# Optimization experiments

Measured on AMD Instinct MI355X. Metric: run time of the kernel, lower is better.

Reference implementation:

```python
import jax, jax.numpy as jnp
import numpy as np


def _causal_kernel_mask(K):
    # casual_mask[i, K-i:] = 0 for i in 1..p
    p = K // 2
    m = np.ones((p + 1, K), np.float32)
    for i in range(1, p + 1):
        m[i, K - i:] = 0.0
    return jnp.asarray(m)


def setup_inputs() -> dict:
    rng = jax.random.key(0)
    k0, k1, k2, k3, k4 = jax.random.split(rng, 5)
    B, H, N, F = 2, 16, 1024, 64
    V, K = 32000, 5
    return {
        "input_ids": jax.random.randint(k0, (B, N), 0, V),
        "query": jax.random.normal(k1, (B, H, N, F), dtype=jnp.float32),
        "key": jax.random.normal(k2, (B, H, N, F), dtype=jnp.float32),
        "value": jax.random.normal(k3, (B, H, N, F), dtype=jnp.float32),
        "emb_weight": jax.random.normal(k4, (V, 2 * K), dtype=jnp.float32) * 0.02,
    }


def reference(input_ids, query, key, value, emb_weight):
    B, H, N, F = query.shape
    K = emb_weight.shape[1] // 2  # head/layer invariant -> emb dim = 2*K
    p = K // 2
    G = 2 * H

    # ---- get_kernel (layer 0; head_invariant + layer_invariant) ----
    kern = emb_weight[input_ids]                       # [B,N,2K]
    kern = kern.reshape(B, N, 2, 1, K)                 # [B,N,2,1,K]
    kern = jnp.broadcast_to(kern, (B, N, 2, H, K)).reshape(B, N, G, K)

    # ---- conv_key_value (for_casual=True, strict_on_casual=True) ----
    kv = jnp.concatenate([key, value], axis=1)         # [B,2H,N,F]
    kv_pad = jnp.pad(kv, ((0, 0), (0, 0), (p, p), (0, 0)))
    # unfold over token dim: [B,2H,K,N,F]
    kv_unf = jnp.stack([kv_pad[:, :, k:k + N, :] for k in range(K)], axis=2)
    cmask = _causal_kernel_mask(K)                     # [p+1,K]
    kern_m = kern[:, :, :, None, :] * cmask[None, None, None]  # [B,N,2H,p+1,K]
    # dynamic depthwise conv with per-offset causal masking
    out = jnp.einsum('bgknf,bngjk->bgjnf', kv_unf, kern_m)     # [B,2H,p+1,N,F]
    key_c = out[:, :H, 0]                              # [B,H,N,F]
    value_c = out[:, H:, 0]                            # [B,H,N,F]

    # ---- attention with causal-boundary corrections (n_past = 0) ----
    scale = 1.0 / jnp.sqrt(jnp.asarray(F, dtype=query.dtype))
    q = query * scale
    scores = jnp.einsum('bhnf,bhmf->bhnm', q, key_c)   # [B,H,N,N]

    # correct_attn_weights_near_casual_boundary
    for i in range(p):
        off = p - 1 - i
        cb_key = out[:, :H, 1 + i]                     # [B,H,N,F]
        corr = jnp.einsum('bhnf,bhnf->bhn', q[:, :, off:, :], cb_key[:, :, :N - off, :])
        rows = jnp.arange(N - off) + off
        cols = jnp.arange(N - off)
        scores = scores.at[:, :, rows, cols].set(corr)

    causal = jnp.tril(jnp.ones((N, N), dtype=bool))
    scores = jnp.where(causal, scores, jnp.asarray(-1e9, dtype=scores.dtype))
    probs = jax.nn.softmax(scores, axis=-1)
    attn = jnp.einsum('bhnm,bhmf->bhnf', probs, value_c)

    # correct_attn_output_near_casual_boundary
    for i in range(p):
        off = p - 1 - i
        cb_value = out[:, H:, 1 + i]                   # [B,H,N,F]
        idx = jnp.arange(N - off)
        diag_w = probs[:, :, idx + off, idx]           # diag offset=-off: [B,H,N-off]
        diff_v = cb_value[:, :, :N - off, :] - value_c[:, :, :N - off, :]
        diff = diag_w[..., None] * diff_v
        attn = attn + jnp.pad(diff, ((0, 0), (0, 0), (off, 0), (0, 0)))

    return attn
```

## Files before the change

### kernel.cpp

```cpp
#include <hip/hip_runtime.h>

#define HD    64
#define NSEQ  1024
#define NPB   12
#define CROWS 32
#define LOG2E 1.44269504088896f

typedef __attribute__((ext_vector_type(8))) __bf16 bf16x8;
typedef __attribute__((ext_vector_type(4))) float  f32x4;
typedef __attribute__((ext_vector_type(4))) unsigned short u16x4;

__device__ __constant__ unsigned char PAIRS12[NPB] = {
    6, 8, 10, 12, 14, 15, 4, 13, 2, 11, 0, 9 };

__device__ inline unsigned short f2bf(float x) {
    unsigned u = __float_as_uint(x);
    return (unsigned short)((u + 0x7fffu + ((u >> 16) & 1u)) >> 16);
}
__device__ inline unsigned pk2(float a, float b) {
    return (unsigned)f2bf(a) | ((unsigned)f2bf(b) << 16);
}
__device__ inline float dot4(f32x4 a, f32x4 b) {
    return a.x * b.x + a.y * b.y + a.z * b.z + a.w * b.w;
}

__global__ __launch_bounds__(256) void conv_kernel(
    const int* __restrict__ ids,
    const float* __restrict__ keyg,
    const float* __restrict__ valg,
    const float* __restrict__ qg,
    const float* __restrict__ emb,
    unsigned short* __restrict__ kc,
    unsigned short* __restrict__ vcT,
    float* __restrict__ dg1, float* __restrict__ dg2)
{
    __shared__ float se[(CROWS + 1) * 10];
    __shared__ float vtile[CROWS][68];
    int pid = blockIdx.x;
    int bh = pid & 31;
    int n0 = (pid >> 5) * CROWS;
    int b  = bh >> 4;
    int t  = threadIdx.x;
    size_t hb = (size_t)bh * NSEQ * HD;

    for (int u = t; u < (CROWS + 1) * 10; u += 256) {
        int r = u / 10, c = u - r * 10;
        int n = n0 - 1 + r;
        se[u] = (n >= 0) ? emb[(size_t)ids[b * NSEQ + n] * 10 + c] : 0.f;
    }
    __syncthreads();

    const float* kb = keyg + hb;
    const float* vb = valg + hb;
#pragma unroll
    for (int i = 0; i < 2; ++i) {
        int u  = (i << 8) + t;
        int nl = u >> 4, g4 = u & 15;
        int n  = n0 + nl, f = g4 << 2;
        const float* e  = se + (nl + 1) * 10;
        const float* ep = se + nl * 10;
        f32x4 xk[5], xv[5];
#pragma unroll
        for (int k = 0; k < 5; ++k) {
            int m = n + k - 2;
            if (m >= 0 && m < NSEQ) {
                xk[k] = *(const f32x4*)(kb + (size_t)m * HD + f);
                xv[k] = *(const f32x4*)(vb + (size_t)m * HD + f);
            } else {
                xk[k] = (f32x4){0.f, 0.f, 0.f, 0.f};
                xv[k] = (f32x4){0.f, 0.f, 0.f, 0.f};
            }
        }
        f32x4 km3 = (n >= 3) ? *(const f32x4*)(kb + (size_t)(n - 3) * HD + f)
                             : (f32x4){0.f, 0.f, 0.f, 0.f};
        f32x4 qv = *(const f32x4*)(qg + hb + (size_t)n * HD + f) * (0.125f * LOG2E);

        f32x4 k012 = e[0] * xk[0] + e[1] * xk[1] + e[2] * xk[2];
        f32x4 kcv  = k012 + e[3] * xk[3] + e[4] * xk[4];
        f32x4 vcv  = e[5] * xv[0] + e[6] * xv[1] + e[7] * xv[2] + e[8] * xv[3] + e[9] * xv[4];

        u16x4 kq;
        kq.x = f2bf(kcv.x); kq.y = f2bf(kcv.y); kq.z = f2bf(kcv.z); kq.w = f2bf(kcv.w);
        *(u16x4*)(kc + hb + (size_t)n * HD + f) = kq;
        *(f32x4*)(&vtile[nl][f]) = vcv;

        float s2 = dot4(qv, k012);
        f32x4 kj1 = ep[0] * km3 + ep[1] * xk[0] + ep[2] * xk[1] + ep[3] * xk[2];
        float s1 = dot4(qv, kj1);
#pragma unroll
        for (int o = 1; o < 16; o <<= 1) {
            s2 += __shfl_xor(s2, o, 64);
            s1 += __shfl_xor(s1, o, 64);
        }
        if (g4 == 0) {
            dg2[bh * NSEQ + n] = s2;
            dg1[bh * NSEQ + n] = s1;
        }
    }
    __syncthreads();
#pragma unroll
    for (int i = 0; i < 2; ++i) {
        int u = (i << 8) + t;
        int f = u >> 3, nn = (u & 7) << 2;
        u16x4 o;
        o.x = f2bf(vtile[nn + 0][f]);
        o.y = f2bf(vtile[nn + 1][f]);
        o.z = f2bf(vtile[nn + 2][f]);
        o.w = f2bf(vtile[nn + 3][f]);
        *(u16x4*)(vcT + ((size_t)bh * HD + f) * NSEQ + n0 + nn) = o;
    }
}

__global__ __launch_bounds__(512, 4) void attn_kernel(
    const float* __restrict__ qg,
    const unsigned short* __restrict__ kc,
    const unsigned short* __restrict__ vcT,
    const float* __restrict__ dg1, const float* __restrict__ dg2,
    const float* __restrict__ valg, const int* __restrict__ ids,
    const float* __restrict__ emb,
    float* __restrict__ pML, unsigned short* __restrict__ pO,
    float* __restrict__ outg)
{
    __shared__ __align__(16) unsigned char sK[2][8192];
    __shared__ __align__(16) unsigned char sV[2][8192];
    __shared__ __align__(16) unsigned char sP[16384];

    int pid  = blockIdx.x;
    int bh   = pid & 31;
    int slot = pid >> 5;
    int code = PAIRS12[slot];
    int jj = code >> 1, cch = code & 1;
    int t0 = cch << 3;
    int ntile = 2 * jj + 2;
    int len = cch ? (ntile - 8) : (ntile > 8 ? 8 : ntile);

    int t = threadIdx.x;
    int wv = t >> 6, l = t & 63;
    int w_in = wv & 3;
    int my_j = 2 * jj + (wv >> 2);
    int nc  = (my_j >= 8) ? 2 : 1;
    int lq = l & 15, h = l >> 4, l7 = l & 7;
    int lid = h * 16 + lq;
    int qbw = my_j * 64 + w_in * 16;
    size_t hb = (size_t)bh * NSEQ * HD;

    const unsigned short* kcb = kc  + hb;
    const unsigned short* vtb = vcT + (size_t)bh * HD * NSEQ;

    bf16x8 qb0, qb1;
    {
        const float* qr = qg + hb + (size_t)(qbw + lq) * HD + 8 * h;
        f32x4 a0 = *(const f32x4*)(qr);
        f32x4 a1 = *(const f32x4*)(qr + 4);
        f32x4 b0 = *(const f32x4*)(qr + 32);
        f32x4 b1 = *(const f32x4*)(qr + 36);
        const float S = 0.125f * LOG2E;
        union { unsigned u[4]; bf16x8 v; } u0, u1;
        u0.u[0] = pk2(a0.x * S, a0.y * S); u0.u[1] = pk2(a0.z * S, a0.w * S);
        u0.u[2] = pk2(a1.x * S, a1.y * S); u0.u[3] = pk2(a1.z * S, a1.w * S);
        u1.u[0] = pk2(b0.x * S, b0.y * S); u1.u[1] = pk2(b0.z * S, b0.w * S);
        u1.u[2] = pk2(b1.x * S, b1.y * S); u1.u[3] = pk2(b1.z * S, b1.w * S);
        qb0 = u0.v; qb1 = u1.v;
    }
    float diag2_l = dg2[bh * NSEQ + qbw + lq];
    float diag1_l = dg1[bh * NSEQ + qbw + lq];

    f32x4 of[4];
#pragma unroll
    for (int ft = 0; ft < 4; ++ft) of[ft] = (f32x4){0.f, 0.f, 0.f, 0.f};
    float m_run = -1e30f, denom = 0.f;

    const int ka_off0 = ((0 + h) ^ l7) << 4;
    const int ka_off1 = ((4 + h) ^ l7) << 4;
    const int pr_base = wv * 2048 + lq * 128;
    const int chk0 = ((qbw > 0 ? qbw - 1 : 0) >> 6);

    const int s_r0 = (t & 511) >> 3, s_c0 = t & 7;
    const int s_cs0 = s_c0 ^ (s_r0 & 7);
    const int s_buf0 = t >> 9;
    const int s_r1 = ((t + 512) & 511) >> 3, s_c1 = (t + 512) & 7;
    const int s_cs1 = s_c1 ^ (s_r1 & 7);
    const int s_buf1 = (t + 512) >> 9;

    uint4 pf[2];
    auto issue = [&](int tg) {
        int kv0 = tg << 6;
        pf[0] = (s_buf0 == 0)
            ? *(const uint4*)(kcb + (size_t)(kv0 + s_r0) * HD + s_cs0 * 8)
            : *(const uint4*)(vtb + (size_t)s_r0 * NSEQ + kv0 + s_cs0 * 8);
        pf[1] = (s_buf1 == 0)
            ? *(const uint4*)(kcb + (size_t)(kv0 + s_r1) * HD + s_cs1 * 8)
            : *(const uint4*)(vtb + (size_t)s_r1 * NSEQ + kv0 + s_cs1 * 8);
    };
    auto commit = [&](int cu) {
        *(uint4*)((s_buf0 ? sV[cu] : sK[cu]) + s_r0 * 128 + s_c0 * 16) = pf[0];
        *(uint4*)((s_buf1 ? sV[cu] : sK[cu]) + s_r1 * 128 + s_c1 * 16) = pf[1];
    };

    issue(t0); commit(0);
    if (len > 1) issue(t0 + 1);
    __syncthreads();

    for (int ti = 0; ti < len; ++ti) {
        int cur = ti & 1;
        if (ti + 1 < len) commit(cur ^ 1);
        if (ti + 2 < len) issue(t0 + ti + 2);
        int tg  = t0 + ti;
        int kv0 = tg << 6;
        bool act = (tg <= my_j);

        if (act) {
            const unsigned char* sKc = sK[cur];
            const unsigned char* sVc = sV[cur];
            f32x4 p[4];
            __builtin_amdgcn_s_setprio(1);
#pragma unroll
            for (int st = 0; st < 4; ++st) {
                bf16x8 ka0 = *(const bf16x8*)(sKc + st * 2048 + lq * 128 + ka_off0);
                bf16x8 ka1 = *(const bf16x8*)(sKc + st * 2048 + lq * 128 + ka_off1);
                f32x4 d = (f32x4){0.f, 0.f, 0.f, 0.f};
                d = __builtin_amdgcn_mfma_f32_16x16x32_bf16(ka0, qb0, d, 0, 0, 0);
                d = __builtin_amdgcn_mfma_f32_16x16x32_bf16(ka1, qb1, d, 0, 0, 0);
                p[st] = d;
            }
            __builtin_amdgcn_s_setprio(0);

            if (tg >= chk0) {
                int n_l = qbw + lq;
#pragma unroll
                for (int st = 0; st < 4; ++st)
#pragma unroll
                    for (int r = 0; r < 4; ++r) {
                        int kv = kv0 + st * 16 + 4 * h + r;
                        float dd = p[st][r];
                        if (kv > n_l)           dd = -1e30f;
                        else if (kv == n_l)     dd = diag2_l;
                        else if (kv == n_l - 1) dd = diag1_l;
                        p[st][r] = dd;
                    }
            }

            float tmax = -1e30f;
#pragma unroll
            for (int st = 0; st < 4; ++st)
#pragma unroll
                for (int r = 0; r < 4; ++r) tmax = fmaxf(tmax, p[st][r]);
            tmax = fmaxf(tmax, __shfl_xor(tmax, 16, 64));
            tmax = fmaxf(tmax, __shfl_xor(tmax, 32, 64));
            if (!__all(tmax <= m_run + 7.0f)) {
                float m_new = fmaxf(m_run, tmax);
                float alpha = __builtin_exp2f(m_run - m_new);
                denom *= alpha;
                m_run = m_new;
#pragma unroll
                for (int r = 0; r < 4; ++r) {
                    float ar = __shfl(alpha, 4 * h + r, 64);
                    of[0][r] *= ar; of[1][r] *= ar; of[2][r] *= ar; of[3][r] *= ar;
                }
            }
            float lsum = 0.f;
#pragma unroll
            for (int st = 0; st < 4; ++st)
#pragma unroll
                for (int r = 0; r < 4; ++r) {
                    float e = __builtin_exp2f(p[st][r] - m_run);
                    p[st][r] = e;
                    lsum += e;
                }
            lsum += __shfl_xor(lsum, 16, 64);
            lsum += __shfl_xor(lsum, 32, 64);
            denom += lsum;

#pragma unroll
            for (int st = 0; st < 4; ++st) {
                uint2 uu;
                uu.x = pk2(p[st][0], p[st][1]);
                uu.y = pk2(p[st][2], p[st][3]);
                int chunk = (st << 1) + (h >> 1);
                *(uint2*)(sP + pr_base + ((chunk ^ l7) << 4) + ((h & 1) << 3)) = uu;
            }
            asm volatile("s_waitcnt lgkmcnt(0)" ::: "memory");
            __builtin_amdgcn_sched_barrier(0);

            __builtin_amdgcn_s_setprio(1);
#pragma unroll
            for (int kk = 0; kk < 2; ++kk) {
                int koff = kk ? ka_off1 : ka_off0;
                bf16x8 pa = *(const bf16x8*)(sP + pr_base + koff);
#pragma unroll
                for (int ft = 0; ft < 4; ++ft) {
                    bf16x8 vb = *(const bf16x8*)(sVc + ft * 2048 + lq * 128 + koff);
                    of[ft] = __builtin_amdgcn_mfma_f32_16x16x32_bf16(pa, vb, of[ft], 0, 0, 0);
                }
            }
            __builtin_amdgcn_s_setprio(0);
        }
        if (ti + 1 < len) __syncthreads();
    }

    int psBase = ((bh << 4) | my_j) << 2;
    if (nc > 1) {
        if (h == 0) {
            float2 ml; ml.x = m_run; ml.y = denom;
            *(float2*)(pML + ((size_t)(psBase + cch) * 64 + w_in * 16 + lq) * 2) = ml;
        }
#pragma unroll
        for (int ft = 0; ft < 4; ++ft)
#pragma unroll
            for (int r = 0; r < 4; ++r)
                pO[(size_t)((((psBase + cch) * 4 + w_in) * 4 + ft) * 4 + r) * 64 + lid] =
                    f2bf(of[ft][r]);
        return;
    }

    const float* vraw = valg + hb;
    float* outr = outg + hb;
    const int* idb = ids + (size_t)(bh >> 4) * NSEQ;
#pragma unroll
    for (int r = 0; r < 4; ++r) {
        int qrow = 4 * h + r;
        int n = qbw + qrow;
        float dn = __shfl(denom,   qrow, 64);
        float mf = __shfl(m_run,   qrow, 64);
        float d2 = __shfl(diag2_l, qrow, 64);
        float d1 = __shfl(diag1_l, qrow, 64);
        float inv = 1.0f / dn;
        float p2 = __builtin_exp2f(d2 - mf) * inv;
        float p1 = (n >= 1) ? __builtin_exp2f(d1 - mf) * inv : 0.f;
        int id_n = idb[n];
        float e8  = emb[(size_t)id_n * 10 + 8];
        float e9  = emb[(size_t)id_n * 10 + 9];
        float e9p = (n >= 1) ? emb[(size_t)idb[n - 1] * 10 + 9] : 0.f;
        float ca = -(p2 * e8 + p1 * e9p);
        float cb = -p2 * e9;
#pragma unroll
        for (int ft = 0; ft < 4; ++ft) {
            int f = ft * 16 + lq;
            float v = of[ft][r] * inv;
            if (n + 1 < NSEQ) v += ca * vraw[(size_t)(n + 1) * HD + f];
            if (n + 2 < NSEQ) v += cb * vraw[(size_t)(n + 2) * HD + f];
            outr[(size_t)n * HD + f] = v;
        }
    }
}

__global__ __launch_bounds__(256) void merge_kernel(
    const float* __restrict__ pML, const unsigned short* __restrict__ pO,
    const float* __restrict__ dg1, const float* __restrict__ dg2,
    const float* __restrict__ valg, const int* __restrict__ ids,
    const float* __restrict__ emb, float* __restrict__ outg)
{
    int pid = blockIdx.x;
    int bh = pid & 31, j = (pid >> 5) + 8;
    int t = threadIdx.x;
    int rloc = t >> 2, fg = t & 3;
    int n = (j << 6) + rloc;
    int f0 = fg << 4;
    size_t hb = (size_t)bh * NSEQ * HD;
    int psBase = ((bh << 4) | j) << 2;

    float mc[2], lc[2];
#pragma unroll
    for (int c = 0; c < 2; ++c) {
        float2 v = *(const float2*)(pML + ((size_t)(psBase + c) * 64 + rloc) * 2);
        mc[c] = v.x; lc[c] = v.y;
    }
    float mg = fmaxf(mc[0], mc[1]);
    float D = 0.f;
    f32x4 a0 = (f32x4){0.f,0.f,0.f,0.f}, a1 = a0, a2 = a0, a3 = a0;
#pragma unroll
    for (int c = 0; c < 2; ++c) {
        float wc = __builtin_exp2f(mc[c] - mg);
        D += lc[c] * wc;
        const unsigned short* pp = pO +
            (size_t)((((psBase + c) * 4 + (rloc >> 4)) * 4 + fg) * 4 + (rloc & 3)) * 64
            + ((rloc >> 2) & 3) * 16;
        uint4 ua = *(const uint4*)(pp);
        uint4 ub = *(const uint4*)(pp + 8);
        a0.x += wc * __uint_as_float(ua.x << 16);
        a0.y += wc * __uint_as_float(ua.x & 0xffff0000u);
        a0.z += wc * __uint_as_float(ua.y << 16);
        a0.w += wc * __uint_as_float(ua.y & 0xffff0000u);
        a1.x += wc * __uint_as_float(ua.z << 16);
        a1.y += wc * __uint_as_float(ua.z & 0xffff0000u);
        a1.z += wc * __uint_as_float(ua.w << 16);
        a1.w += wc * __uint_as_float(ua.w & 0xffff0000u);
        a2.x += wc * __uint_as_float(ub.x << 16);
        a2.y += wc * __uint_as_float(ub.x & 0xffff0000u);
        a2.z += wc * __uint_as_float(ub.y << 16);
        a2.w += wc * __uint_as_float(ub.y & 0xffff0000u);
        a3.x += wc * __uint_as_float(ub.z << 16);
        a3.y += wc * __uint_as_float(ub.z & 0xffff0000u);
        a3.z += wc * __uint_as_float(ub.w << 16);
        a3.w += wc * __uint_as_float(ub.w & 0xffff0000u);
    }
    float inv = 1.0f / D;
    float d2 = dg2[bh * NSEQ + n], d1 = dg1[bh * NSEQ + n];
    float p2 = __builtin_exp2f(d2 - mg) * inv;
    float p1 = __builtin_exp2f(d1 - mg) * inv;
    const int* idb = ids + (size_t)(bh >> 4) * NSEQ;
    int id_n = idb[n];
    float e8  = emb[(size_t)id_n * 10 + 8];
    float e9  = emb[(size_t)id_n * 10 + 9];
    float e9p = emb[(size_t)idb[n - 1] * 10 + 9];
    float ca = -(p2 * e8 + p1 * e9p);
    float cb = -p2 * e9;

    a0 *= inv; a1 *= inv; a2 *= inv; a3 *= inv;
    if (n + 1 < NSEQ) {
        const float* v1 = valg + hb + (size_t)(n + 1) * HD + f0;
        a0 += ca * *(const f32x4*)(v1);
        a1 += ca * *(const f32x4*)(v1 + 4);
        a2 += ca * *(const f32x4*)(v1 + 8);
        a3 += ca * *(const f32x4*)(v1 + 12);
    }
    if (n + 2 < NSEQ) {
        const float* v2 = valg + hb + (size_t)(n + 2) * HD + f0;
        a0 += cb * *(const f32x4*)(v2);
        a1 += cb * *(const f32x4*)(v2 + 4);
        a2 += cb * *(const f32x4*)(v2 + 8);
        a3 += cb * *(const f32x4*)(v2 + 12);
    }
    float* o = outg + hb + (size_t)n * HD + f0;
    *(f32x4*)(o)      = a0;
    *(f32x4*)(o + 4)  = a1;
    *(f32x4*)(o + 8)  = a2;
    *(f32x4*)(o + 12) = a3;
}

extern "C" void kernel_launch(void* const* d_in, const int* in_sizes, int n_in,
                              void* d_out, int out_size, void* d_ws, size_t ws_size,
                              hipStream_t stream)
{
    const int*   ids = (const int*)  d_in[0];
    const float* q   = (const float*)d_in[1];
    const float* key = (const float*)d_in[2];
    const float* val = (const float*)d_in[3];
    const float* emb = (const float*)d_in[4];
    float* out = (float*)d_out;

    char* w = (char*)d_ws;
    unsigned short* kc  = (unsigned short*)(w);
    unsigned short* vcT = (unsigned short*)(w + (4u << 20));
    float* dg1 = (float*)(w + 8388608);
    float* dg2 = (float*)(w + 8519680);
    float* pML = (float*)(w + 8650752);
    unsigned short* pO = (unsigned short*)(w + 9699328);

    conv_kernel<<<1024, 256, 0, stream>>>(ids, key, val, q, emb, kc, vcT, dg1, dg2);
    attn_kernel<<<32 * NPB, 512, 0, stream>>>(q, kc, vcT, dg1, dg2, val, ids, emb,
                                              pML, pO, out);
    merge_kernel<<<256, 256, 0, stream>>>(pML, pO, dg1, dg2, val, ids, emb, out);
}
```

Before: 54.84 us.

## Stage key/value halo tiles in shared memory and widen conv blocks to 64 rows

The conv kernel now loads each block's 64-row key and value tile, plus a 3-row halo, into shared memory once. The 5-tap convolution then reads its neighbours from LDS instead of issuing up to six redundant global loads per row. Blocks cover 64 rows instead of 32, so the grid is halved and halo overhead is amortised. In exchange the kernel uses more LDS (about 40KB per block), has fewer blocks, and adds an extra barrier to reuse the key buffer for the value transpose.

```diff
diff --git a/kernel.cpp b/kernel.cpp
--- a/kernel.cpp
+++ b/kernel.cpp
@@ -3,7 +3,6 @@
 #define HD    64
 #define NSEQ  1024
 #define NPB   12
-#define CROWS 32
 #define LOG2E 1.44269504088896f
 
 typedef __attribute__((ext_vector_type(8))) __bf16 bf16x8;
@@ -34,58 +33,72 @@
     unsigned short* __restrict__ vcT,
     float* __restrict__ dg1, float* __restrict__ dg2)
 {
-    __shared__ float se[(CROWS + 1) * 10];
-    __shared__ float vtile[CROWS][68];
+    __shared__ __align__(16) float sA[70 * 68];
+    __shared__ __align__(16) float sB[70 * 68];
+    __shared__ float sE[65 * 10];
+
     int pid = blockIdx.x;
     int bh = pid & 31;
-    int n0 = (pid >> 5) * CROWS;
+    int n0 = (pid >> 5) << 6;
     int b  = bh >> 4;
     int t  = threadIdx.x;
     size_t hb = (size_t)bh * NSEQ * HD;
-
-    for (int u = t; u < (CROWS + 1) * 10; u += 256) {
+    const float* kb = keyg + hb;
+    const float* vb = valg + hb;
+
+    for (int u = t; u < 650; u += 256) {
         int r = u / 10, c = u - r * 10;
         int n = n0 - 1 + r;
-        se[u] = (n >= 0) ? emb[(size_t)ids[b * NSEQ + n] * 10 + c] : 0.f;
+        sE[u] = (n >= 0) ? emb[(size_t)ids[b * NSEQ + n] * 10 + c] : 0.f;
+    }
+    for (int u = t; u < 70 * 16; u += 256) {
+        int r = u >> 4, f = (u & 15) << 2;
+        int g = n0 - 3 + r;
+        f32x4 kv4 = (f32x4){0.f, 0.f, 0.f, 0.f};
+        f32x4 vv4 = (f32x4){0.f, 0.f, 0.f, 0.f};
+        if (g >= 0 && g < NSEQ) {
+            kv4 = *(const f32x4*)(kb + (size_t)g * HD + f);
+            vv4 = *(const f32x4*)(vb + (size_t)g * HD + f);
+        }
+        *(f32x4*)(sA + r * 68 + f) = kv4;
+        *(f32x4*)(sB + r * 68 + f) = vv4;
     }
     __syncthreads();
 
-    const float* kb = keyg + hb;
-    const float* vb = valg + hb;
-#pragma unroll
-    for (int i = 0; i < 2; ++i) {
+    f32x4 vcv_save[4];
+#pragma unroll
+    for (int i = 0; i < 4; ++i) {
         int u  = (i << 8) + t;
         int nl = u >> 4, g4 = u & 15;
         int n  = n0 + nl, f = g4 << 2;
-        const float* e  = se + (nl + 1) * 10;
-        const float* ep = se + nl * 10;
-        f32x4 xk[5], xv[5];
-#pragma unroll
-        for (int k = 0; k < 5; ++k) {
-            int m = n + k - 2;
-            if (m >= 0 && m < NSEQ) {
-                xk[k] = *(const f32x4*)(kb + (size_t)m * HD + f);
-                xv[k] = *(const f32x4*)(vb + (size_t)m * HD + f);
-            } else {
-                xk[k] = (f32x4){0.f, 0.f, 0.f, 0.f};
-                xv[k] = (f32x4){0.f, 0.f, 0.f, 0.f};
-            }
-        }
-        f32x4 km3 = (n >= 3) ? *(const f32x4*)(kb + (size_t)(n - 3) * HD + f)
-                             : (f32x4){0.f, 0.f, 0.f, 0.f};
+        const float* e  = sE + (nl + 1) * 10;
+        const float* ep = sE + nl * 10;
+        const float* ar = sA + nl * 68 + f;
+        const float* br = sB + nl * 68 + f;
+        f32x4 km3 = *(const f32x4*)(ar);
+        f32x4 x0 = *(const f32x4*)(ar + 68);
+        f32x4 x1 = *(const f32x4*)(ar + 2 * 68);
+        f32x4 x2 = *(const f32x4*)(ar + 3 * 68);
+        f32x4 x3 = *(const f32x4*)(ar + 4 * 68);
+        f32x4 x4 = *(const f32x4*)(ar + 5 * 68);
+        f32x4 v0 = *(const f32x4*)(br + 68);
+        f32x4 v1 = *(const f32x4*)(br + 2 * 68);
+        f32x4 v2 = *(const f32x4*)(br + 3 * 68);
+        f32x4 v3 = *(const f32x4*)(br + 4 * 68);
+        f32x4 v4 = *(const f32x4*)(br + 5 * 68);
         f32x4 qv = *(const f32x4*)(qg + hb + (size_t)n * HD + f) * (0.125f * LOG2E);
 
-        f32x4 k012 = e[0] * xk[0] + e[1] * xk[1] + e[2] * xk[2];
-        f32x4 kcv  = k012 + e[3] * xk[3] + e[4] * xk[4];
-        f32x4 vcv  = e[5] * xv[0] + e[6] * xv[1] + e[7] * xv[2] + e[8] * xv[3] + e[9] * xv[4];
+        f32x4 k012 = e[0] * x0 + e[1] * x1 + e[2] * x2;
+        f32x4 kcv  = k012 + e[3] * x3 + e[4] * x4;
+        f32x4 vcv  = e[5] * v0 + e[6] * v1 + e[7] * v2 + e[8] * v3 + e[9] * v4;
 
         u16x4 kq;
         kq.x = f2bf(kcv.x); kq.y = f2bf(kcv.y); kq.z = f2bf(kcv.z); kq.w = f2bf(kcv.w);
         *(u16x4*)(kc + hb + (size_t)n * HD + f) = kq;
-        *(f32x4*)(&vtile[nl][f]) = vcv;
+        vcv_save[i] = vcv;
 
         float s2 = dot4(qv, k012);
-        f32x4 kj1 = ep[0] * km3 + ep[1] * xk[0] + ep[2] * xk[1] + ep[3] * xk[2];
+        f32x4 kj1 = ep[0] * km3 + ep[1] * x0 + ep[2] * x1 + ep[3] * x2;
         float s1 = dot4(qv, kj1);
 #pragma unroll
         for (int o = 1; o < 16; o <<= 1) {
@@ -98,15 +111,23 @@
         }
     }
     __syncthreads();
-#pragma unroll
-    for (int i = 0; i < 2; ++i) {
+    float* vt = sA;
+#pragma unroll
+    for (int i = 0; i < 4; ++i) {
         int u = (i << 8) + t;
-        int f = u >> 3, nn = (u & 7) << 2;
+        int nl = u >> 4, f = (u & 15) << 2;
+        *(f32x4*)(vt + nl * 68 + f) = vcv_save[i];
+    }
+    __syncthreads();
+#pragma unroll
+    for (int i = 0; i < 4; ++i) {
+        int u = (i << 8) + t;
+        int f = u >> 4, nn = (u & 15) << 2;
         u16x4 o;
-        o.x = f2bf(vtile[nn + 0][f]);
-        o.y = f2bf(vtile[nn + 1][f]);
-        o.z = f2bf(vtile[nn + 2][f]);
-        o.w = f2bf(vtile[nn + 3][f]);
+        o.x = f2bf(vt[(nn + 0) * 68 + f]);
+        o.y = f2bf(vt[(nn + 1) * 68 + f]);
+        o.z = f2bf(vt[(nn + 2) * 68 + f]);
+        o.w = f2bf(vt[(nn + 3) * 68 + f]);
         *(u16x4*)(vcT + ((size_t)bh * HD + f) * NSEQ + n0 + nn) = o;
     }
 }
@@ -447,7 +468,7 @@
     float* pML = (float*)(w + 8650752);
     unsigned short* pO = (unsigned short*)(w + 9699328);
 
-    conv_kernel<<<1024, 256, 0, stream>>>(ids, key, val, q, emb, kc, vcT, dg1, dg2);
+    conv_kernel<<<512, 256, 0, stream>>>(ids, key, val, q, emb, kc, vcT, dg1, dg2);
     attn_kernel<<<32 * NPB, 512, 0, stream>>>(q, kc, vcT, dg1, dg2, val, ids, emb,
                                               pML, pO, out);
     merge_kernel<<<256, 256, 0, stream>>>(pML, pO, dg1, dg2, val, ids, emb, out);
```

Measured after the change: 50.51 us. -7.9%, faster.
